# Performance work log

Measured on AMD Instinct MI355X. Metric: run time of the kernel, lower is better.

Reference implementation:

```python
import jax, jax.numpy as jnp
import numpy as np

T, B, C, H, W = 9, 8, 256, 56, 56


def setup_inputs() -> dict:
    key = jax.random.key(0)
    k1, k2, k3, k4 = jax.random.split(key, 4)
    feature_maps_sequence = jax.random.normal(k1, (T, B, C, H, W), dtype=jnp.float32)
    # Conv2d(2C, 1, kernel_size=1): weight [1, 2C, 1, 1], bias [1]
    w = jax.random.normal(k2, (1, 2 * C, 1, 1), dtype=jnp.float32) * 0.02
    b = jax.random.normal(k3, (1,), dtype=jnp.float32) * 0.02
    gamma = jax.random.normal(k4, (1,), dtype=jnp.float32)
    return {"feature_maps_sequence": feature_maps_sequence, "w": w, "b": b, "gamma": gamma}


def reference(feature_maps_sequence, w, b, gamma):
    seq = feature_maps_sequence  # [T, B, C, H, W]
    t = seq.shape[0]
    center = seq[t // 2]  # [B, C, H, W]
    c = seq.shape[2]
    # 1x1 conv over concat([center, frame]) == dot with split weight halves + bias
    w_center = w[0, :c, 0, 0]  # [C]
    w_other = w[0, c:, 0, 0]   # [C]
    score_center = jnp.einsum('bchw,c->bhw', center, w_center)          # [B, H, W]
    score_other = jnp.einsum('tbchw,c->tbhw', seq, w_other)             # [T, B, H, W]
    scores = score_center[None] + score_other + b[0]                    # [T, B, H, W]
    attn = jax.nn.softmax(scores, axis=0)                               # softmax over T
    attended = jnp.einsum('tbhw,tbchw->bchw', attn, seq)                # [B, C, H, W]
    return center + gamma * attended
```

## Files before the change

### kernel.cpp

```cpp
#include <hip/hip_runtime.h>
#include <math.h>

#define TT 9
#define BN 8
#define CC 256
#define HW 3136
#define P 8
#define NCHUNK (HW / P)
#define CENTER_T 4

__global__ __launch_bounds__(256) void fused_stage_kernel(
    const float* __restrict__ seq, const float* __restrict__ w,
    const float* __restrict__ gamma, float* __restrict__ out) {
  int blk = blockIdx.x;
  int b = blk & 7;
  int chunk = blk >> 3;
  int px0 = chunk * P;
  int tid = threadIdx.x;

  __shared__ __align__(16) float tile[TT * CC * P];
  __shared__ float wsh[CC];
  __shared__ float red[TT * P * 4];
  __shared__ __align__(16) float sc[TT * P];

  wsh[tid] = w[CC + tid];

  {
    const float* sb = seq + px0;
    #pragma unroll
    for (int k = 0; k < 18; ++k) {
      int i = k * 256 + tid;
      int t = i >> 9;
      int r = i & 511;
      int c = r >> 1;
      int g = (r & 1) * 4;
      float4 v = *(const float4*)(sb + (((size_t)t * BN + b) * CC + c) * HW + g);
      *(float4*)(&tile[(t * CC + c) * P + g]) = v;
    }
  }
  __syncthreads();

  for (int v = tid; v < 288; v += 256) {
    int pair = v >> 2;
    int cp = v & 3;
    int t = pair >> 3;
    int px = pair & 7;
    int c0 = cp * 64;
    float a = 0.f;
    #pragma unroll
    for (int i = 0; i < 64; ++i)
      a = fmaf(tile[(t * CC + c0 + i) * P + px], wsh[c0 + i], a);
    red[pair * 4 + cp] = a;
  }
  __syncthreads();

  if (tid < P) {
    float vv[TT];
    float m = -1e30f;
    #pragma unroll
    for (int t = 0; t < TT; ++t) {
      int pr = (t * P + tid) * 4;
      float s = red[pr] + red[pr + 1] + red[pr + 2] + red[pr + 3];
      vv[t] = s;
      m = fmaxf(m, s);
    }
    float s = 0.f;
    #pragma unroll
    for (int t = 0; t < TT; ++t) { vv[t] = __expf(vv[t] - m); s += vv[t]; }
    float inv = 1.f / s;
    #pragma unroll
    for (int t = 0; t < TT; ++t) sc[t * P + tid] = vv[t] * inv;
  }
  __syncthreads();

  {
    int c = tid;
    float4 o0 = {0.f, 0.f, 0.f, 0.f}, o1 = {0.f, 0.f, 0.f, 0.f};
    float4 c0v = {0.f, 0.f, 0.f, 0.f}, c1v = {0.f, 0.f, 0.f, 0.f};
    #pragma unroll
    for (int t = 0; t < TT; ++t) {
      float4 s0 = *(const float4*)(&sc[t * P]);
      float4 s1 = *(const float4*)(&sc[t * P + 4]);
      const float4* tp = (const float4*)(&tile[(t * CC + c) * P]);
      float4 v0 = tp[0], v1 = tp[1];
      o0.x = fmaf(s0.x, v0.x, o0.x);
      o0.y = fmaf(s0.y, v0.y, o0.y);
      o0.z = fmaf(s0.z, v0.z, o0.z);
      o0.w = fmaf(s0.w, v0.w, o0.w);
      o1.x = fmaf(s1.x, v1.x, o1.x);
      o1.y = fmaf(s1.y, v1.y, o1.y);
      o1.z = fmaf(s1.z, v1.z, o1.z);
      o1.w = fmaf(s1.w, v1.w, o1.w);
      if (t == CENTER_T) { c0v = v0; c1v = v1; }
    }
    float gm = gamma[0];
    float4 r0, r1;
    r0.x = fmaf(gm, o0.x, c0v.x);
    r0.y = fmaf(gm, o0.y, c0v.y);
    r0.z = fmaf(gm, o0.z, c0v.z);
    r0.w = fmaf(gm, o0.w, c0v.w);
    r1.x = fmaf(gm, o1.x, c1v.x);
    r1.y = fmaf(gm, o1.y, c1v.y);
    r1.z = fmaf(gm, o1.z, c1v.z);
    r1.w = fmaf(gm, o1.w, c1v.w);
    float* ob = out + ((size_t)b * CC + c) * HW + px0;
    *(float4*)(ob) = r0;
    *(float4*)(ob + 4) = r1;
  }
}

extern "C" void kernel_launch(void* const* d_in, const int* in_sizes, int n_in,
                              void* d_out, int out_size, void* d_ws, size_t ws_size,
                              hipStream_t stream) {
  const float* seq = (const float*)d_in[0];
  const float* w = (const float*)d_in[1];
  const float* gamma = (const float*)d_in[3];
  float* out = (float*)d_out;

  fused_stage_kernel<<<BN * NCHUNK, 256, 0, stream>>>(seq, w, gamma, out);
}
```

Before: 344.4 us.

## Use persistent blocks with register prefetch of the next pixel chunk and swizzled LDS

Replaces the one-block-per-chunk launch with a persistent grid of 512 blocks, each looping over pixel chunks. The next chunk's 18 float4 values are loaded into registers while the current chunk is computed, so global loads overlap compute. The LDS tile is XOR-swizzled to cut bank conflicts, and custom barriers wait only on LDS counters. In exchange, register pressure rises from holding 72 prefetch floats, and fewer blocks are resident to hide latency.

After: 434.1 us. +26.0%, slower.

```diff
diff --git a/kernel.cpp b/kernel.cpp
--- a/kernel.cpp
+++ b/kernel.cpp
@@ -7,16 +7,24 @@
 #define HW 3136
 #define P 8
 #define NCHUNK (HW / P)
+#define ITEMS (BN * NCHUNK)
+#define GRID 512
 #define CENTER_T 4
 
-__global__ __launch_bounds__(256) void fused_stage_kernel(
+#define BAR_LGKM()                                        \
+  do {                                                    \
+    __builtin_amdgcn_sched_barrier(0);                    \
+    asm volatile("s_waitcnt lgkmcnt(0)" ::: "memory");    \
+    __builtin_amdgcn_s_barrier();                         \
+    __builtin_amdgcn_sched_barrier(0);                    \
+  } while (0)
+
+__global__ __launch_bounds__(256, 2) void fused_pipe_kernel(
     const float* __restrict__ seq, const float* __restrict__ w,
     const float* __restrict__ gamma, float* __restrict__ out) {
-  int blk = blockIdx.x;
-  int b = blk & 7;
-  int chunk = blk >> 3;
-  int px0 = chunk * P;
-  int tid = threadIdx.x;
+  const int bid = blockIdx.x;
+  const int b = bid & 7;
+  const int tid = threadIdx.x;
 
   __shared__ __align__(16) float tile[TT * CC * P];
   __shared__ float wsh[CC];
@@ -24,88 +32,119 @@
   __shared__ __align__(16) float sc[TT * P];
 
   wsh[tid] = w[CC + tid];
+  const float gm = gamma[0];
 
-  {
-    const float* sb = seq + px0;
-    #pragma unroll
+  const int c_lo = tid >> 1;
+  const int g = (tid & 1) * 4;
+  const int fsw = ((c_lo >> 2) & 7) << 2;
+  const int wbase = (8 * c_lo + g) ^ fsw;
+  const float* sgb = seq + (size_t)b * CC * HW + (size_t)c_lo * HW + g;
+
+  int px0 = (bid >> 3) * P;
+  const int nit = (bid < (ITEMS % GRID)) ? (ITEMS / GRID + 1) : (ITEMS / GRID);
+
+  float4 pre[18];
+#pragma unroll
+  for (int k = 0; k < 18; ++k) {
+    const int koff = (k >> 1) * (BN * CC * HW) + (k & 1) * (128 * HW);
+    pre[k] = *(const float4*)(sgb + koff + px0);
+  }
+
+  for (int it = 0; it < nit; ++it) {
+#pragma unroll
     for (int k = 0; k < 18; ++k) {
-      int i = k * 256 + tid;
-      int t = i >> 9;
-      int r = i & 511;
-      int c = r >> 1;
-      int g = (r & 1) * 4;
-      float4 v = *(const float4*)(sb + (((size_t)t * BN + b) * CC + c) * HW + g);
-      *(float4*)(&tile[(t * CC + c) * P + g]) = v;
+      *(float4*)(&tile[wbase + (k >> 1) * 2048 + (k & 1) * 1024]) = pre[k];
     }
-  }
-  __syncthreads();
+    if (it + 1 < nit) {
+      const int px0n = px0 + (GRID / BN) * P;
+#pragma unroll
+      for (int k = 0; k < 18; ++k) {
+        const int koff = (k >> 1) * (BN * CC * HW) + (k & 1) * (128 * HW);
+        pre[k] = *(const float4*)(sgb + koff + px0n);
+      }
+    }
+    BAR_LGKM();
 
-  for (int v = tid; v < 288; v += 256) {
-    int pair = v >> 2;
-    int cp = v & 3;
-    int t = pair >> 3;
-    int px = pair & 7;
-    int c0 = cp * 64;
-    float a = 0.f;
-    #pragma unroll
-    for (int i = 0; i < 64; ++i)
-      a = fmaf(tile[(t * CC + c0 + i) * P + px], wsh[c0 + i], a);
-    red[pair * 4 + cp] = a;
-  }
-  __syncthreads();
+    {
+      const int pair = tid >> 2, cp = tid & 3;
+      const int t = pair >> 3, px = pair & 7;
+      const int sbase = (t * CC + cp) * P + px;
+      float a = 0.f;
+#pragma unroll
+      for (int i = 0; i < 64; ++i)
+        a = fmaf(tile[(sbase ^ ((i & 7) << 2)) + 32 * i], wsh[cp + 4 * i], a);
+      red[tid] = a;
+      if (tid < 32) {
+        const int cp2 = tid & 3;
+        const int px2 = ((tid + 256) >> 2) & 7;
+        const int sbase2 = (8 * CC + cp2) * P + px2;
+        float a2 = 0.f;
+#pragma unroll
+        for (int i = 0; i < 64; ++i)
+          a2 = fmaf(tile[(sbase2 ^ ((i & 7) << 2)) + 32 * i], wsh[cp2 + 4 * i], a2);
+        red[tid + 256] = a2;
+      }
+    }
+    BAR_LGKM();
 
-  if (tid < P) {
-    float vv[TT];
-    float m = -1e30f;
-    #pragma unroll
-    for (int t = 0; t < TT; ++t) {
-      int pr = (t * P + tid) * 4;
-      float s = red[pr] + red[pr + 1] + red[pr + 2] + red[pr + 3];
-      vv[t] = s;
-      m = fmaxf(m, s);
+    if (tid < P) {
+      float vv[TT];
+      float m = -1e30f;
+#pragma unroll
+      for (int t = 0; t < TT; ++t) {
+        const int pr = (t * P + tid) * 4;
+        const float s = red[pr] + red[pr + 1] + red[pr + 2] + red[pr + 3];
+        vv[t] = s;
+        m = fmaxf(m, s);
+      }
+      float s = 0.f;
+#pragma unroll
+      for (int t = 0; t < TT; ++t) { vv[t] = __expf(vv[t] - m); s += vv[t]; }
+      const float inv = 1.f / s;
+#pragma unroll
+      for (int t = 0; t < TT; ++t) sc[t * P + tid] = vv[t] * inv;
     }
-    float s = 0.f;
-    #pragma unroll
-    for (int t = 0; t < TT; ++t) { vv[t] = __expf(vv[t] - m); s += vv[t]; }
-    float inv = 1.f / s;
-    #pragma unroll
-    for (int t = 0; t < TT; ++t) sc[t * P + tid] = vv[t] * inv;
-  }
-  __syncthreads();
+    BAR_LGKM();
 
-  {
-    int c = tid;
-    float4 o0 = {0.f, 0.f, 0.f, 0.f}, o1 = {0.f, 0.f, 0.f, 0.f};
-    float4 c0v = {0.f, 0.f, 0.f, 0.f}, c1v = {0.f, 0.f, 0.f, 0.f};
-    #pragma unroll
-    for (int t = 0; t < TT; ++t) {
-      float4 s0 = *(const float4*)(&sc[t * P]);
-      float4 s1 = *(const float4*)(&sc[t * P + 4]);
-      const float4* tp = (const float4*)(&tile[(t * CC + c) * P]);
-      float4 v0 = tp[0], v1 = tp[1];
-      o0.x = fmaf(s0.x, v0.x, o0.x);
-      o0.y = fmaf(s0.y, v0.y, o0.y);
-      o0.z = fmaf(s0.z, v0.z, o0.z);
-      o0.w = fmaf(s0.w, v0.w, o0.w);
-      o1.x = fmaf(s1.x, v1.x, o1.x);
-      o1.y = fmaf(s1.y, v1.y, o1.y);
-      o1.z = fmaf(s1.z, v1.z, o1.z);
-      o1.w = fmaf(s1.w, v1.w, o1.w);
-      if (t == CENTER_T) { c0v = v0; c1v = v1; }
+    {
+      const int c = tid;
+      const int f2 = ((c >> 2) & 7) << 2;
+      const int abase0 = (8 * c) ^ f2;
+      const int abase4 = (8 * c + 4) ^ f2;
+      float4 o0 = {0.f, 0.f, 0.f, 0.f}, o1 = {0.f, 0.f, 0.f, 0.f};
+      float4 c0v = {0.f, 0.f, 0.f, 0.f}, c1v = {0.f, 0.f, 0.f, 0.f};
+#pragma unroll
+      for (int t = 0; t < TT; ++t) {
+        const float4 s0 = *(const float4*)(&sc[t * P]);
+        const float4 s1 = *(const float4*)(&sc[t * P + 4]);
+        const float4 v0 = *(const float4*)(&tile[abase0 + t * 2048]);
+        const float4 v1 = *(const float4*)(&tile[abase4 + t * 2048]);
+        o0.x = fmaf(s0.x, v0.x, o0.x);
+        o0.y = fmaf(s0.y, v0.y, o0.y);
+        o0.z = fmaf(s0.z, v0.z, o0.z);
+        o0.w = fmaf(s0.w, v0.w, o0.w);
+        o1.x = fmaf(s1.x, v1.x, o1.x);
+        o1.y = fmaf(s1.y, v1.y, o1.y);
+        o1.z = fmaf(s1.z, v1.z, o1.z);
+        o1.w = fmaf(s1.w, v1.w, o1.w);
+        if (t == CENTER_T) { c0v = v0; c1v = v1; }
+      }
+      float4 r0, r1;
+      r0.x = fmaf(gm, o0.x, c0v.x);
+      r0.y = fmaf(gm, o0.y, c0v.y);
+      r0.z = fmaf(gm, o0.z, c0v.z);
+      r0.w = fmaf(gm, o0.w, c0v.w);
+      r1.x = fmaf(gm, o1.x, c1v.x);
+      r1.y = fmaf(gm, o1.y, c1v.y);
+      r1.z = fmaf(gm, o1.z, c1v.z);
+      r1.w = fmaf(gm, o1.w, c1v.w);
+      float* ob = out + ((size_t)b * CC + c) * HW + px0;
+      *(float4*)(ob) = r0;
+      *(float4*)(ob + 4) = r1;
     }
-    float gm = gamma[0];
-    float4 r0, r1;
-    r0.x = fmaf(gm, o0.x, c0v.x);
-    r0.y = fmaf(gm, o0.y, c0v.y);
-    r0.z = fmaf(gm, o0.z, c0v.z);
-    r0.w = fmaf(gm, o0.w, c0v.w);
-    r1.x = fmaf(gm, o1.x, c1v.x);
-    r1.y = fmaf(gm, o1.y, c1v.y);
-    r1.z = fmaf(gm, o1.z, c1v.z);
-    r1.w = fmaf(gm, o1.w, c1v.w);
-    float* ob = out + ((size_t)b * CC + c) * HW + px0;
-    *(float4*)(ob) = r0;
-    *(float4*)(ob + 4) = r1;
+
+    px0 += (GRID / BN) * P;
+    BAR_LGKM();
   }
 }
 
@@ -117,5 +156,5 @@
   const float* gamma = (const float*)d_in[3];
   float* out = (float*)d_out;
 
-  fused_stage_kernel<<<BN * NCHUNK, 256, 0, stream>>>(seq, w, gamma, out);
+  fused_pipe_kernel<<<GRID, 256, 0, stream>>>(seq, w, gamma, out);
 }
```
